# Optimization experiments

Measured on AMD Instinct MI355X. Metric: run time of the kernel, lower is better.

The kernel has to match this reference:

```python
import jax, jax.numpy as jnp
import numpy as np

HEAD_NUM = 16
MASK_FILL = 100000.0  # source uses +1e5 on masked entries (not -inf)


def setup_inputs() -> dict:
    key = jax.random.key(0)
    k1, k2, k3, k4, k5 = jax.random.split(key, 5)
    B, S, E = 2, 2048, 1024
    scale = 0.02
    return {
        "x": jax.random.normal(k1, (B, S, E), dtype=jnp.float32),
        "W_atten": jax.random.normal(k2, (E, 3 * E), dtype=jnp.float32) * scale,
        "b_atten": jax.random.normal(k3, (3 * E,), dtype=jnp.float32) * scale,
        "W_proj": jax.random.normal(k4, (E, E), dtype=jnp.float32) * scale,
        "b_proj": jax.random.normal(k5, (E,), dtype=jnp.float32) * scale,
    }


def reference(x, W_atten, b_atten, W_proj, b_proj):
    B, S, E = x.shape
    H = HEAD_NUM
    hd = E // H
    # QKV projection: [B, S, 3E]
    qkv = x @ W_atten + b_atten
    # reshape [B, S, H, 3*hd] -> [B, H, S, 3*hd], chunk into q,k,v [B,H,S,hd]
    qkv = jnp.transpose(qkv.reshape(B, S, H, 3 * hd), (0, 2, 1, 3))
    q, k, v = jnp.split(qkv, 3, axis=-1)
    # raw scores, NO 1/sqrt(dk) scaling (faithful to source)
    w = jnp.einsum("bhqd,bhkd->bhqk", q, k)
    # causal mask applied as w*mask + (1-mask)*1e5 (faithful to source)
    mask = jnp.tril(jnp.ones((S, S), dtype=w.dtype))
    w = w * mask + (1.0 - mask) * MASK_FILL
    # softmax over dim=1 == HEAD axis (faithful to source quirk)
    w = jax.nn.softmax(w, axis=1)
    # attn_drop: identity in eval mode
    a = jnp.einsum("bhqk,bhkd->bhqd", w, v)  # [B,H,S,hd]
    a = jnp.transpose(a, (0, 2, 1, 3)).reshape(B, S, E)
    h = a @ W_proj + b_proj
    # resi_drop: identity in eval mode
    return h
```

## Files before the change

### kernel.cpp

```cpp
#include <hip/hip_runtime.h>

#define DI __device__ __forceinline__

typedef __attribute__((ext_vector_type(8))) short s16x8;
typedef __attribute__((ext_vector_type(4))) short s16x4;
typedef __attribute__((ext_vector_type(4))) float f32x4;

DI unsigned short f2bf(float f){
  unsigned u = __float_as_uint(f);
  u = (u + 0x7FFFu + ((u >> 16) & 1u)) >> 16;
  return (unsigned short)u;
}
DI float bf2f(unsigned short h){
  return __uint_as_float(((unsigned)h) << 16);
}
DI float exp2i(float x){ float r; asm("v_exp_f32 %0, %1" : "=v"(r) : "v"(x)); return r; }

DI void gll16(const void* g, void* l){
  __builtin_amdgcn_global_load_lds((const __attribute__((address_space(1))) void*)g,
                                   (__attribute__((address_space(3))) void*)l, 16, 0, 0);
}

#define VMCNT(n) asm volatile("s_waitcnt vmcnt(" #n ")" ::: "memory")
#define SB() __builtin_amdgcn_sched_barrier(0)

__global__ void prep_kernel(const float* __restrict__ x, unsigned short* __restrict__ xb,
                            const float* __restrict__ Wa, unsigned short* __restrict__ WaT,
                            const float* __restrict__ Wp, unsigned short* __restrict__ WpT)
{
  __shared__ float t[32][33];
  int blk = blockIdx.x, tid = threadIdx.x;
  if (blk < 2048){
    int i = blk * 256 + tid;
    const float4* p = (const float4*)x + (size_t)i * 2;
    float4 a = p[0], b = p[1];
    s16x8 o;
    o[0] = (short)f2bf(a.x); o[1] = (short)f2bf(a.y); o[2] = (short)f2bf(a.z); o[3] = (short)f2bf(a.w);
    o[4] = (short)f2bf(b.x); o[5] = (short)f2bf(b.y); o[6] = (short)f2bf(b.z); o[7] = (short)f2bf(b.w);
    ((s16x8*)xb)[i] = o;
  } else {
    const float* in; unsigned short* out; int R, C, bx, by;
    if (blk < 5120){
      int k = blk - 2048; in = Wa; out = WaT; R = 1024; C = 3072; bx = k % 96; by = k / 96;
    } else {
      int k = blk - 5120; in = Wp; out = WpT; R = 1024; C = 1024; bx = k % 32; by = k / 32;
    }
    int c0 = bx * 32, r0 = by * 32;
    int tx = tid & 31, ty = tid >> 5;
    #pragma unroll
    for (int i = 0; i < 4; i++)
      t[ty + i*8][tx] = in[(size_t)(r0 + ty + i*8) * C + c0 + tx];
    __syncthreads();
    #pragma unroll
    for (int i = 0; i < 4; i++)
      out[(size_t)(c0 + ty + i*8) * R + r0 + tx] = f2bf(t[tx][ty + i*8]);
  }
}

template<int MODE, int BM>
__launch_bounds__(256)
__global__ void gemm_kernel(const unsigned short* __restrict__ A,
                            const unsigned short* __restrict__ Wt,
                            const float* __restrict__ bias,
                            int N,
                            unsigned short* __restrict__ qb,
                            unsigned short* __restrict__ kb,
                            unsigned short* __restrict__ vt,
                            float* __restrict__ out)
{
  constexpr int MI = BM / 32;
  constexpr int AC = BM / 32;
  const int K = 1024;
  __shared__ __align__(16) unsigned short Sm[BM*64 + 128*64];
  unsigned short* As = Sm;
  unsigned short* Bs = Sm + BM*64;

  int lin = blockIdx.y * gridDim.x + blockIdx.x;
  int chunk = (gridDim.x * gridDim.y) >> 3;
  int v = (lin & 7) * chunk + (lin >> 3);
  int bx = v % gridDim.x, by = v / gridDim.x;
  int m0 = by * BM, n0 = bx * 128;

  int tid = threadIdx.x;
  int lane = tid & 63, w = tid >> 6;
  int row_l = lane & 15, kgrp = lane >> 4;
  int wm = (w >> 1) * (MI * 16), wn = (w & 1) * 64;

  const unsigned short* asrc[AC];
  const unsigned short* bsrc[4];
  int ldsoA[AC], ldsoB[4];
  int chnk = (lane & 7) ^ (lane >> 3);
  #pragma unroll
  for (int c4 = 0; c4 < AC; c4++){
    int r = c4*32 + w*8 + (lane >> 3);
    asrc[c4] = A + (size_t)(m0 + r) * K + chnk*8;
    ldsoA[c4] = (c4*32 + w*8) * 64;
  }
  #pragma unroll
  for (int c4 = 0; c4 < 4; c4++){
    int r = c4*32 + w*8 + (lane >> 3);
    bsrc[c4] = Wt + (size_t)(n0 + r) * K + chnk*8;
    ldsoB[c4] = (c4*32 + w*8) * 64;
  }
  int eA[MI], eB[4];
  #pragma unroll
  for (int i = 0; i < MI; i++){
    int ra = wm + i*16 + row_l;
    eA[i] = (ra*64 + kgrp*8) ^ ((ra & 7) << 3);
  }
  #pragma unroll
  for (int i = 0; i < 4; i++){
    int rb = wn + i*16 + row_l;
    eB[i] = (rb*64 + kgrp*8) ^ ((rb & 7) << 3);
  }

  f32x4 acc[MI][4];
  #pragma unroll
  for (int i = 0; i < MI; i++)
    #pragma unroll
    for (int j = 0; j < 4; j++)
      acc[i][j] = (f32x4){0.f, 0.f, 0.f, 0.f};

  for (int k0 = 0; k0 < K; k0 += 64){
    #pragma unroll
    for (int c4 = 0; c4 < AC; c4++)
      gll16(asrc[c4] + k0, (void*)(As + ldsoA[c4]));
    #pragma unroll
    for (int c4 = 0; c4 < 4; c4++)
      gll16(bsrc[c4] + k0, (void*)(Bs + ldsoB[c4]));
    __syncthreads();
    #pragma unroll
    for (int kc = 0; kc < 2; kc++){
      s16x8 af[MI], bfr[4];
      #pragma unroll
      for (int mi = 0; mi < MI; mi++)
        af[mi] = *(const s16x8*)&As[eA[mi] ^ (kc*32)];
      #pragma unroll
      for (int ni = 0; ni < 4; ni++)
        bfr[ni] = *(const s16x8*)&Bs[eB[ni] ^ (kc*32)];
      #pragma unroll
      for (int mi = 0; mi < MI; mi++)
        #pragma unroll
        for (int ni = 0; ni < 4; ni++)
          acc[mi][ni] = __builtin_amdgcn_mfma_f32_16x16x32_bf16(af[mi], bfr[ni], acc[mi][ni], 0, 0, 0);
    }
    __syncthreads();
  }

  if (MODE == 0){
    constexpr int WU = BM / 4;
    constexpr int SWM = BM / 16 - 1;
    unsigned long long* ldsT = (unsigned long long*)Sm;
    #pragma unroll
    for (int mi = 0; mi < MI; mi++){
      #pragma unroll
      for (int ni = 0; ni < 4; ni++){
        int np = wn + ni*16 + row_l;
        int gc = n0 + np;
        int hh = gc / 192, cc = gc % 192;
        float bia = bias[gc];
        if (cc < 128){
          #pragma unroll
          for (int j = 0; j < 4; j++){
            int gr = m0 + wm + mi*16 + kgrp*4 + j;
            float v2 = acc[mi][ni][j] + bia;
            if (cc < 64){
              qb[(size_t)gr * 1024 + hh*64 + cc] = f2bf(v2 * 1.44269504f);
            } else {
              int d = cc - 64; int b = gr >> 11, s = gr & 2047;
              int kt = s >> 6, kk = s & 63;
              kb[(size_t)((b*16 + hh)*32 + kt) * 4096 + ((kk*64 + d) ^ ((kk & 7) << 3))] = f2bf(v2);
            }
          }
        } else {
          float v0 = acc[mi][ni][0] + bia, v1 = acc[mi][ni][1] + bia;
          float v2 = acc[mi][ni][2] + bia, v3 = acc[mi][ni][3] + bia;
          unsigned lo, hi;
          asm("v_cvt_pk_bf16_f32 %0, %1, %2" : "=v"(lo) : "v"(v0), "v"(v1));
          asm("v_cvt_pk_bf16_f32 %0, %1, %2" : "=v"(hi) : "v"(v2), "v"(v3));
          int mq = (wm + mi*16 + kgrp*4) >> 2;
          ldsT[np*WU + (mq ^ ((np & SWM) << 2))] = ((unsigned long long)hi << 32) | (unsigned long long)lo;
        }
      }
    }
    __syncthreads();
    constexpr int SUBS = BM / 64;
    constexpr int ITEMS = 128 * SUBS * 8;
    int bb = m0 >> 11, s_base = m0 & 2047;
    for (int item = tid; item < ITEMS; item += 256){
      int np = item / (SUBS * 8);
      int rem = item - np * (SUBS * 8);
      int sub = rem >> 3;
      int c = rem & 7;
      int gcv = n0 + np;
      int cc = gcv % 192;
      if (cc < 128) continue;
      int d = cc - 128, hh = gcv / 192;
      int mq0 = sub*16 + c*2;
      s16x8 val = *(const s16x8*)&Sm[np*BM + ((mq0 ^ ((np & SWM) << 2)) << 2)];
      size_t base = ((size_t)((bb*16 + hh)*32) + (s_base >> 6) + sub) * 4096 + d*64 + ((c ^ (d & 7)) << 3);
      *(s16x8*)&vt[base] = val;
    }
  } else {
    #pragma unroll
    for (int mi = 0; mi < MI; mi++){
      #pragma unroll
      for (int ni = 0; ni < 4; ni++){
        #pragma unroll
        for (int j = 0; j < 4; j++){
          int gr = m0 + wm + mi*16 + kgrp*4 + j;
          int gc = n0 + wn + ni*16 + row_l;
          out[(size_t)gr * N + gc] = acc[mi][ni][j] + bias[gc];
        }
      }
    }
  }
}

__global__ void sufv_kernel(const unsigned short* __restrict__ vt, float* __restrict__ sufv){
  __shared__ float tot[4][64];
  int bh = blockIdx.x;
  int tid = threadIdx.x;
  int tq = tid >> 6, d = tid & 63;
  const unsigned short* base = vt + (size_t)bh * 32 * 4096;
  float s[8];
  float run = 0.f;
  for (int j = 7; j >= 0; j--){
    int t = tq*8 + j;
    float rs = 0.f;
    #pragma unroll
    for (int c = 0; c < 8; c++){
      int idx = (d*64 + c*8) ^ ((d & 7) << 3);
      s16x8 v = *(const s16x8*)&base[(size_t)t*4096 + idx];
      #pragma unroll
      for (int e = 0; e < 8; e++) rs += bf2f((unsigned short)v[e]);
    }
    run += rs; s[j] = run;
  }
  tot[tq][d] = run;
  __syncthreads();
  float carry = 0.f;
  for (int t2 = tq+1; t2 < 4; t2++) carry += tot[t2][d];
  #pragma unroll
  for (int j = 0; j < 8; j++)
    sufv[((size_t)bh*33 + tq*8 + j)*64 + d] = s[j] + carry;
  if (tid < 64) sufv[((size_t)bh*33 + 32)*64 + tid] = 0.f;
}

__launch_bounds__(256)
__global__ void dpass_kernel(const unsigned short* __restrict__ qbuf,
                             const unsigned short* __restrict__ kb,
                             unsigned short* __restrict__ invb)
{
  __shared__ unsigned short Kst[4][4096];
  int bid = blockIdx.x;
  int blk = (bid & 7) * 132 + (bid >> 3);
  int b = blk / 528, t0 = blk % 528;
  int kt = (int)(32.5f - sqrtf(1056.25f - 2.f*t0));
  while (kt*(65-kt)/2 > t0) kt--;
  while ((kt+1)*(64-kt)/2 <= t0) kt++;
  int qt = kt + (t0 - kt*(65-kt)/2);

  int tid = threadIdx.x, lane = tid & 63, w = tid >> 6;
  int row_l = lane & 15, kgrp = lane >> 4;

  const unsigned short* ktb = kb + ((size_t)(b*16)*32 + kt) * 4096;
  int sgoff = (w*128 + lane)*8;

  auto stage = [&](int hh){
    const unsigned short* src = ktb + (size_t)hh * 131072;
    gll16(src + sgoff,       (void*)(&Kst[hh & 3][0] + w*1024));
    gll16(src + sgoff + 512, (void*)(&Kst[hh & 3][0] + w*1024 + 512));
  };

  int e0[4];
  #pragma unroll
  for (int ks = 0; ks < 4; ks++){
    int row = ks*16 + row_l;
    e0[ks] = (row*64 + kgrp*8) ^ ((row & 7) << 3);
  }

  const unsigned short* qrow_p = qbuf + (size_t)(b*2048 + qt*64 + w*16 + row_l) * 1024;

  stage(0); stage(1);
  s16x8 qa0 = *(const s16x8*)&qrow_p[kgrp*8];
  s16x8 qa1 = *(const s16x8*)&qrow_p[32 + kgrp*8];
  s16x8 qb0 = *(const s16x8*)&qrow_p[64 + kgrp*8];
  s16x8 qb1 = *(const s16x8*)&qrow_p[64 + 32 + kgrp*8];
  SB();

  f32x4 esum[4];
  #pragma unroll
  for (int ks = 0; ks < 4; ks++) esum[ks] = (f32x4){0.f,0.f,0.f,0.f};

  for (int t = 0; t < 8; t++){
    int h = 2*t;
    s16x8 qn0, qn1, qn2, qn3;
    if (t < 7){
      qn0 = *(const s16x8*)&qrow_p[(h+2)*64 + kgrp*8];
      qn1 = *(const s16x8*)&qrow_p[(h+2)*64 + 32 + kgrp*8];
      qn2 = *(const s16x8*)&qrow_p[(h+3)*64 + kgrp*8];
      qn3 = *(const s16x8*)&qrow_p[(h+3)*64 + 32 + kgrp*8];
    }
    SB();
    if (t == 0)     VMCNT(8);
    else if (t < 7) VMCNT(4);
    else            VMCNT(0);
    SB();
    __builtin_amdgcn_s_barrier();
    SB();
    if (t < 7){ stage(h+2); stage(h+3); }
    SB();

    const unsigned short* kl0 = &Kst[h & 3][0];
    const unsigned short* kl1 = &Kst[(h+1) & 3][0];
    #pragma unroll
    for (int ks = 0; ks < 4; ks++){
      s16x8 a0 = *(const s16x8*)&kl0[e0[ks]];
      s16x8 a1 = *(const s16x8*)&kl0[e0[ks] ^ 32];
      f32x4 sc = __builtin_amdgcn_mfma_f32_16x16x32_bf16(a0, qa0, (f32x4){0.f,0.f,0.f,0.f}, 0, 0, 0);
      sc = __builtin_amdgcn_mfma_f32_16x16x32_bf16(a1, qa1, sc, 0, 0, 0);
      s16x8 b0 = *(const s16x8*)&kl1[e0[ks]];
      s16x8 b1 = *(const s16x8*)&kl1[e0[ks] ^ 32];
      f32x4 sd = __builtin_amdgcn_mfma_f32_16x16x32_bf16(b0, qb0, (f32x4){0.f,0.f,0.f,0.f}, 0, 0, 0);
      sd = __builtin_amdgcn_mfma_f32_16x16x32_bf16(b1, qb1, sd, 0, 0, 0);
      #pragma unroll
      for (int j = 0; j < 4; j++) esum[ks][j] += exp2i(sc[j]) + exp2i(sd[j]);
    }
    if (t < 7){ qa0 = qn0; qa1 = qn1; qb0 = qn2; qb1 = qn3; }
  }

  int qcol = qt*64 + w*16 + row_l;
  unsigned short* dst = invb + (size_t)b*4194304 + (size_t)qcol*2048 + kt*64 + kgrp*4;
  #pragma unroll
  for (int ks = 0; ks < 4; ks++){
    float r0 = 1.f/esum[ks][0], r1 = 1.f/esum[ks][1];
    float r2 = 1.f/esum[ks][2], r3 = 1.f/esum[ks][3];
    unsigned lo, hi;
    asm("v_cvt_pk_bf16_f32 %0, %1, %2" : "=v"(lo) : "v"(r0), "v"(r1));
    asm("v_cvt_pk_bf16_f32 %0, %1, %2" : "=v"(hi) : "v"(r2), "v"(r3));
    uint2 pk; pk.x = lo; pk.y = hi;
    *(uint2*)&dst[ks*16] = pk;
  }
}

__launch_bounds__(256)
__global__ void pv_kernel(const unsigned short* __restrict__ qbuf,
                          const unsigned short* __restrict__ kb,
                          const unsigned short* __restrict__ vt,
                          const unsigned short* __restrict__ invb,
                          const float* __restrict__ sufv,
                          unsigned short* __restrict__ ab)
{
  __shared__ unsigned short Kst[3][4096];
  __shared__ unsigned short Vst[2][4096];
  __shared__ unsigned short Wsh[4][1152];

  int bid = blockIdx.x;
  int blk = ((bid & 7) << 6) | (bid >> 3);
  int i = blk & 15;
  int h = (blk >> 4) & 15;
  int b = blk >> 8;

  int tid = threadIdx.x, lane = tid & 63, w = tid >> 6;
  int row_l = lane & 15, kgrp = lane >> 4;

  const unsigned short* KT = kb + (size_t)((b*16 + h)*32) * 4096;
  const unsigned short* VT = vt + (size_t)((b*16 + h)*32) * 4096;
  int sgoff = (w*128 + lane)*8;
  unsigned short* Wsw = &Wsh[w][0];

  int eK[4];
  #pragma unroll
  for (int ks = 0; ks < 4; ks++){
    int row = ks*16 + row_l;
    eK[ks] = (row*64 + kgrp*8) ^ ((row & 7) << 3);
  }

  auto stageK = [&](int kt, int buf){
    gll16(KT + (size_t)kt*4096 + sgoff,       (void*)(&Kst[buf][0] + w*1024));
    gll16(KT + (size_t)kt*4096 + sgoff + 512, (void*)(&Kst[buf][0] + w*1024 + 512));
  };
  auto stageV = [&](int kt, int buf){
    gll16(VT + (size_t)kt*4096 + sgoff,       (void*)(&Vst[buf][0] + w*1024));
    gll16(VT + (size_t)kt*4096 + sgoff + 512, (void*)(&Vst[buf][0] + w*1024 + 512));
  };

  auto run = [&](int qt, int k1t){
    int q0 = qt * 64;
    int qv = q0 + w*16 + row_l;
    const unsigned short* qrow_p = qbuf + (size_t)(b*2048 + qv) * 1024 + h*64;
    s16x8 qf0 = *(const s16x8*)&qrow_p[kgrp*8];
    s16x8 qf1 = *(const s16x8*)&qrow_p[32 + kgrp*8];
    SB();
    const unsigned short* ivrow = invb + (size_t)b*4194304 + (size_t)qv*2048 + kgrp*4;

    f32x4 pvv[4];
    #pragma unroll
    for (int d = 0; d < 4; d++) pvv[d] = (f32x4){0.f,0.f,0.f,0.f};

    __syncthreads();
    stageK(0, 0);
    stageV(0, 0);
    s16x4 i1[4];
    #pragma unroll
    for (int ks = 0; ks < 4; ks++) i1[ks] = *(const s16x4*)&ivrow[ks*16];
    if (1 < k1t) stageK(1, 1);
    SB();

    for (int kt = 0; kt < k1t; kt++){
      bool nx1 = (kt + 1 < k1t), nx2 = (kt + 2 < k1t);
      bool first = (kt == 0);

      s16x4 icur[4];
      #pragma unroll
      for (int ks = 0; ks < 4; ks++) icur[ks] = i1[ks];
      if (nx1){
        #pragma unroll
        for (int ks = 0; ks < 4; ks++) i1[ks] = *(const s16x4*)&ivrow[(kt+1)*64 + ks*16];
      }
      SB();
      if (first){
        if (nx1) VMCNT(10);
        else     VMCNT(4);
      } else {
        if (nx1) VMCNT(6);
        else     VMCNT(0);
      }
      SB();
      __builtin_amdgcn_s_barrier();
      SB();
      if (nx1) stageV(kt+1, (kt+1) & 1);
      if (nx2) stageK(kt+2, (kt+2) % 3);
      SB();

      const unsigned short* kl = &Kst[kt % 3][0];
      const unsigned short* vl = &Vst[kt & 1][0];
      f32x4 sc[4];
      __builtin_amdgcn_s_setprio(1);
      #pragma unroll
      for (int ks = 0; ks < 4; ks++){
        s16x8 a0 = *(const s16x8*)&kl[eK[ks]];
        s16x8 a1 = *(const s16x8*)&kl[eK[ks] ^ 32];
        sc[ks] = __builtin_amdgcn_mfma_f32_16x16x32_bf16(a0, qf0, (f32x4){0.f,0.f,0.f,0.f}, 0, 0, 0);
        sc[ks] = __builtin_amdgcn_mfma_f32_16x16x32_bf16(a1, qf1, sc[ks], 0, 0, 0);
      }
      __builtin_amdgcn_s_setprio(0);

      if (kt == qt){
        int kbase = kt*64 + kgrp*4;
        #pragma unroll
        for (int ks = 0; ks < 4; ks++){
          #pragma unroll
          for (int j = 0; j < 4; j++){
            float wv = exp2i(sc[ks][j]) * bf2f((unsigned short)icur[ks][j]);
            sc[ks][j] = (kbase + ks*16 + j > qv) ? 0.0625f : wv;
          }
          unsigned lo, hi;
          asm("v_cvt_pk_bf16_f32 %0, %1, %2" : "=v"(lo) : "v"(sc[ks][0]), "v"(sc[ks][1]));
          asm("v_cvt_pk_bf16_f32 %0, %1, %2" : "=v"(hi) : "v"(sc[ks][2]), "v"(sc[ks][3]));
          uint2 pk2; pk2.x = lo; pk2.y = hi;
          *(uint2*)&Wsw[row_l*72 + ks*16 + kgrp*4] = pk2;
        }
      } else {
        #pragma unroll
        for (int ks = 0; ks < 4; ks++){
          #pragma unroll
          for (int j = 0; j < 4; j++)
            sc[ks][j] = exp2i(sc[ks][j]) * bf2f((unsigned short)icur[ks][j]);
          unsigned lo, hi;
          asm("v_cvt_pk_bf16_f32 %0, %1, %2" : "=v"(lo) : "v"(sc[ks][0]), "v"(sc[ks][1]));
          asm("v_cvt_pk_bf16_f32 %0, %1, %2" : "=v"(hi) : "v"(sc[ks][2]), "v"(sc[ks][3]));
          uint2 pk2; pk2.x = lo; pk2.y = hi;
          *(uint2*)&Wsw[row_l*72 + ks*16 + kgrp*4] = pk2;
        }
      }

      __builtin_amdgcn_s_setprio(1);
      #pragma unroll
      for (int kc = 0; kc < 2; kc++){
        s16x8 af = *(const s16x8*)&Wsw[row_l*72 + kc*32 + kgrp*8];
        #pragma unroll
        for (int dq = 0; dq < 4; dq++){
          s16x8 vf = *(const s16x8*)&vl[eK[dq] ^ (kc*32)];
          pvv[dq] = __builtin_amdgcn_mfma_f32_16x16x32_bf16(af, vf, pvv[dq], 0, 0, 0);
        }
      }
      __builtin_amdgcn_s_setprio(0);
    }

    int tsuf = qt + 1;
    #pragma unroll
    for (int dq = 0; dq < 4; dq++){
      int d = dq*16 + row_l;
      float suf = sufv[((size_t)(b*16 + h)*33 + tsuf)*64 + d];
      #pragma unroll
      for (int j = 0; j < 4; j++){
        int qo = q0 + w*16 + kgrp*4 + j;
        ab[(size_t)(b*2048 + qo)*1024 + h*64 + d] = f2bf(pvv[dq][j] + 0.0625f * suf);
      }
    }
  };

  run(i, i + 1);
  run(31 - i, 32 - i);
}

extern "C" void kernel_launch(void* const* d_in, const int* in_sizes, int n_in,
                              void* d_out, int out_size, void* d_ws, size_t ws_size,
                              hipStream_t stream) {
  (void)in_sizes; (void)n_in; (void)out_size; (void)ws_size;
  const float* x  = (const float*)d_in[0];
  const float* Wa = (const float*)d_in[1];
  const float* ba = (const float*)d_in[2];
  const float* Wp = (const float*)d_in[3];
  const float* bp = (const float*)d_in[4];
  float* out = (float*)d_out;

  char* ws = (char*)d_ws;
  size_t off = 0;
  auto alloc = [&](size_t bytes) -> void* {
    void* p = ws + off;
    off += (bytes + 255) & ~(size_t)255;
    return p;
  };
  unsigned short* xb   = (unsigned short*)alloc((size_t)4096*1024*2);
  unsigned short* WaT  = (unsigned short*)alloc((size_t)3072*1024*2);
  unsigned short* WpT  = (unsigned short*)alloc((size_t)1024*1024*2);
  unsigned short* qbuf = (unsigned short*)alloc((size_t)4096*1024*2);
  unsigned short* ktile= (unsigned short*)alloc((size_t)4096*1024*2);
  unsigned short* vtile= (unsigned short*)alloc((size_t)4096*1024*2);
  unsigned short* abuf = (unsigned short*)alloc((size_t)4096*1024*2);
  unsigned short* invb = (unsigned short*)alloc((size_t)2*2048*2048*2);
  float* sufv          = (float*)alloc((size_t)32*33*64*4);

  prep_kernel<<<6144, 256, 0, stream>>>(x, xb, Wa, WaT, Wp, WpT);

  gemm_kernel<0,64><<<dim3(24, 64), 256, 0, stream>>>(xb, WaT, ba, 3072, qbuf, ktile, vtile, nullptr);

  sufv_kernel<<<32, 256, 0, stream>>>(vtile, sufv);

  dpass_kernel<<<1056, 256, 0, stream>>>(qbuf, ktile, invb);

  pv_kernel<<<512, 256, 0, stream>>>(qbuf, ktile, vtile, invb, sufv, abuf);

  gemm_kernel<1,32><<<dim3(8, 128), 256, 0, stream>>>(abuf, WpT, bp, 1024, nullptr, nullptr, nullptr, out);
}
```

Before: 148.3 us.

## Process paired query tiles in one K/V sweep to share staged tiles

Each block previously ran two separate passes over K/V, one for query tile i and one for the mirrored tile 31-i, staging K and V tiles into shared memory twice. The passes are now merged into a single loop over 32-i key tiles. Each staged K/V tile is used by both query tiles while the short tile is still active, which cuts the global-to-LDS traffic and the pipeline restarts. In exchange each thread holds two sets of Q fragments and accumulators, which raises register pressure, and the vmcnt wait counts were retuned to cover the extra inverse-factor loads.

```diff
diff --git a/kernel.cpp b/kernel.cpp
--- a/kernel.cpp
+++ b/kernel.cpp
@@ -386,124 +386,151 @@
     gll16(VT + (size_t)kt*4096 + sgoff + 512, (void*)(&Vst[buf][0] + w*1024 + 512));
   };
 
-  auto run = [&](int qt, int k1t){
-    int q0 = qt * 64;
-    int qv = q0 + w*16 + row_l;
-    const unsigned short* qrow_p = qbuf + (size_t)(b*2048 + qv) * 1024 + h*64;
-    s16x8 qf0 = *(const s16x8*)&qrow_p[kgrp*8];
-    s16x8 qf1 = *(const s16x8*)&qrow_p[32 + kgrp*8];
-    SB();
-    const unsigned short* ivrow = invb + (size_t)b*4194304 + (size_t)qv*2048 + kgrp*4;
-
-    f32x4 pvv[4];
-    #pragma unroll
-    for (int d = 0; d < 4; d++) pvv[d] = (f32x4){0.f,0.f,0.f,0.f};
-
-    __syncthreads();
-    stageK(0, 0);
-    stageV(0, 0);
-    s16x4 i1[4];
-    #pragma unroll
-    for (int ks = 0; ks < 4; ks++) i1[ks] = *(const s16x4*)&ivrow[ks*16];
-    if (1 < k1t) stageK(1, 1);
-    SB();
-
-    for (int kt = 0; kt < k1t; kt++){
-      bool nx1 = (kt + 1 < k1t), nx2 = (kt + 2 < k1t);
-      bool first = (kt == 0);
-
-      s16x4 icur[4];
-      #pragma unroll
-      for (int ks = 0; ks < 4; ks++) icur[ks] = i1[ks];
-      if (nx1){
+  int qtA = i, qtB = 31 - i;
+  int k1t = 32 - i;
+  int qvA = qtA*64 + w*16 + row_l;
+  int qvB = qtB*64 + w*16 + row_l;
+  const unsigned short* qrowA = qbuf + (size_t)(b*2048 + qvA) * 1024 + h*64;
+  const unsigned short* qrowB = qbuf + (size_t)(b*2048 + qvB) * 1024 + h*64;
+  s16x8 qfA0 = *(const s16x8*)&qrowA[kgrp*8];
+  s16x8 qfA1 = *(const s16x8*)&qrowA[32 + kgrp*8];
+  s16x8 qfB0 = *(const s16x8*)&qrowB[kgrp*8];
+  s16x8 qfB1 = *(const s16x8*)&qrowB[32 + kgrp*8];
+  SB();
+  const unsigned short* ivA = invb + (size_t)b*4194304 + (size_t)qvA*2048 + kgrp*4;
+  const unsigned short* ivB = invb + (size_t)b*4194304 + (size_t)qvB*2048 + kgrp*4;
+
+  f32x4 pvA[4], pvB[4];
+  #pragma unroll
+  for (int d = 0; d < 4; d++){ pvA[d] = (f32x4){0.f,0.f,0.f,0.f}; pvB[d] = (f32x4){0.f,0.f,0.f,0.f}; }
+
+  auto compute_tile = [&](int kt, const unsigned short* kl, const unsigned short* vl,
+                          s16x8 qf0, s16x8 qf1, int qt, int qv, s16x4* icur, f32x4* pvv){
+    f32x4 sc[4];
+    __builtin_amdgcn_s_setprio(1);
+    #pragma unroll
+    for (int ks = 0; ks < 4; ks++){
+      s16x8 a0 = *(const s16x8*)&kl[eK[ks]];
+      s16x8 a1 = *(const s16x8*)&kl[eK[ks] ^ 32];
+      sc[ks] = __builtin_amdgcn_mfma_f32_16x16x32_bf16(a0, qf0, (f32x4){0.f,0.f,0.f,0.f}, 0, 0, 0);
+      sc[ks] = __builtin_amdgcn_mfma_f32_16x16x32_bf16(a1, qf1, sc[ks], 0, 0, 0);
+    }
+    __builtin_amdgcn_s_setprio(0);
+    if (kt == qt){
+      int kbase = kt*64 + kgrp*4;
+      #pragma unroll
+      for (int ks = 0; ks < 4; ks++){
         #pragma unroll
-        for (int ks = 0; ks < 4; ks++) i1[ks] = *(const s16x4*)&ivrow[(kt+1)*64 + ks*16];
-      }
-      SB();
-      if (first){
-        if (nx1) VMCNT(10);
-        else     VMCNT(4);
-      } else {
-        if (nx1) VMCNT(6);
-        else     VMCNT(0);
-      }
-      SB();
-      __builtin_amdgcn_s_barrier();
-      SB();
-      if (nx1) stageV(kt+1, (kt+1) & 1);
-      if (nx2) stageK(kt+2, (kt+2) % 3);
-      SB();
-
-      const unsigned short* kl = &Kst[kt % 3][0];
-      const unsigned short* vl = &Vst[kt & 1][0];
-      f32x4 sc[4];
-      __builtin_amdgcn_s_setprio(1);
+        for (int j = 0; j < 4; j++){
+          float wv = exp2i(sc[ks][j]) * bf2f((unsigned short)icur[ks][j]);
+          sc[ks][j] = (kbase + ks*16 + j > qv) ? 0.0625f : wv;
+        }
+        unsigned lo, hi;
+        asm("v_cvt_pk_bf16_f32 %0, %1, %2" : "=v"(lo) : "v"(sc[ks][0]), "v"(sc[ks][1]));
+        asm("v_cvt_pk_bf16_f32 %0, %1, %2" : "=v"(hi) : "v"(sc[ks][2]), "v"(sc[ks][3]));
+        uint2 pk2; pk2.x = lo; pk2.y = hi;
+        *(uint2*)&Wsw[row_l*72 + ks*16 + kgrp*4] = pk2;
+      }
+    } else {
       #pragma unroll
       for (int ks = 0; ks < 4; ks++){
-        s16x8 a0 = *(const s16x8*)&kl[eK[ks]];
-        s16x8 a1 = *(const s16x8*)&kl[eK[ks] ^ 32];
-        sc[ks] = __builtin_amdgcn_mfma_f32_16x16x32_bf16(a0, qf0, (f32x4){0.f,0.f,0.f,0.f}, 0, 0, 0);
-        sc[ks] = __builtin_amdgcn_mfma_f32_16x16x32_bf16(a1, qf1, sc[ks], 0, 0, 0);
-      }
-      __builtin_amdgcn_s_setprio(0);
-
-      if (kt == qt){
-        int kbase = kt*64 + kgrp*4;
         #pragma unroll
-        for (int ks = 0; ks < 4; ks++){
-          #pragma unroll
-          for (int j = 0; j < 4; j++){
-            float wv = exp2i(sc[ks][j]) * bf2f((unsigned short)icur[ks][j]);
-            sc[ks][j] = (kbase + ks*16 + j > qv) ? 0.0625f : wv;
-          }
-          unsigned lo, hi;
-          asm("v_cvt_pk_bf16_f32 %0, %1, %2" : "=v"(lo) : "v"(sc[ks][0]), "v"(sc[ks][1]));
-          asm("v_cvt_pk_bf16_f32 %0, %1, %2" : "=v"(hi) : "v"(sc[ks][2]), "v"(sc[ks][3]));
-          uint2 pk2; pk2.x = lo; pk2.y = hi;
-          *(uint2*)&Wsw[row_l*72 + ks*16 + kgrp*4] = pk2;
-        }
-      } else {
-        #pragma unroll
-        for (int ks = 0; ks < 4; ks++){
-          #pragma unroll
-          for (int j = 0; j < 4; j++)
-            sc[ks][j] = exp2i(sc[ks][j]) * bf2f((unsigned short)icur[ks][j]);
-          unsigned lo, hi;
-          asm("v_cvt_pk_bf16_f32 %0, %1, %2" : "=v"(lo) : "v"(sc[ks][0]), "v"(sc[ks][1]));
-          asm("v_cvt_pk_bf16_f32 %0, %1, %2" : "=v"(hi) : "v"(sc[ks][2]), "v"(sc[ks][3]));
-          uint2 pk2; pk2.x = lo; pk2.y = hi;
-          *(uint2*)&Wsw[row_l*72 + ks*16 + kgrp*4] = pk2;
-        }
-      }
-
-      __builtin_amdgcn_s_setprio(1);
-      #pragma unroll
-      for (int kc = 0; kc < 2; kc++){
-        s16x8 af = *(const s16x8*)&Wsw[row_l*72 + kc*32 + kgrp*8];
-        #pragma unroll
-        for (int dq = 0; dq < 4; dq++){
-          s16x8 vf = *(const s16x8*)&vl[eK[dq] ^ (kc*32)];
-          pvv[dq] = __builtin_amdgcn_mfma_f32_16x16x32_bf16(af, vf, pvv[dq], 0, 0, 0);
-        }
-      }
-      __builtin_amdgcn_s_setprio(0);
-    }
-
-    int tsuf = qt + 1;
+        for (int j = 0; j < 4; j++)
+          sc[ks][j] = exp2i(sc[ks][j]) * bf2f((unsigned short)icur[ks][j]);
+        unsigned lo, hi;
+        asm("v_cvt_pk_bf16_f32 %0, %1, %2" : "=v"(lo) : "v"(sc[ks][0]), "v"(sc[ks][1]));
+        asm("v_cvt_pk_bf16_f32 %0, %1, %2" : "=v"(hi) : "v"(sc[ks][2]), "v"(sc[ks][3]));
+        uint2 pk2; pk2.x = lo; pk2.y = hi;
+        *(uint2*)&Wsw[row_l*72 + ks*16 + kgrp*4] = pk2;
+      }
+    }
+    __builtin_amdgcn_s_setprio(1);
+    #pragma unroll
+    for (int kc = 0; kc < 2; kc++){
+      s16x8 af = *(const s16x8*)&Wsw[row_l*72 + kc*32 + kgrp*8];
+      #pragma unroll
+      for (int dq = 0; dq < 4; dq++){
+        s16x8 vf = *(const s16x8*)&vl[eK[dq] ^ (kc*32)];
+        pvv[dq] = __builtin_amdgcn_mfma_f32_16x16x32_bf16(af, vf, pvv[dq], 0, 0, 0);
+      }
+    }
+    __builtin_amdgcn_s_setprio(0);
+  };
+
+  stageK(0, 0);
+  stageV(0, 0);
+  s16x4 iA1[4], iB1[4];
+  #pragma unroll
+  for (int ks = 0; ks < 4; ks++){
+    iA1[ks] = *(const s16x4*)&ivA[ks*16];
+    iB1[ks] = *(const s16x4*)&ivB[ks*16];
+  }
+  stageK(1, 1);
+  SB();
+
+  for (int kt = 0; kt < k1t; kt++){
+    bool cA  = (kt <= qtA);
+    bool nxA = (kt + 1 <= qtA);
+    bool nx1 = (kt + 1 < k1t), nx2 = (kt + 2 < k1t);
+    bool first = (kt == 0);
+
+    s16x4 icA[4], icB[4];
+    #pragma unroll
+    for (int ks = 0; ks < 4; ks++){ icA[ks] = iA1[ks]; icB[ks] = iB1[ks]; }
+    if (nxA){
+      #pragma unroll
+      for (int ks = 0; ks < 4; ks++) iA1[ks] = *(const s16x4*)&ivA[(kt+1)*64 + ks*16];
+    }
+    if (nx1){
+      #pragma unroll
+      for (int ks = 0; ks < 4; ks++) iB1[ks] = *(const s16x4*)&ivB[(kt+1)*64 + ks*16];
+    }
+    SB();
+    if (first){
+      if (nxA) VMCNT(18);
+      else     VMCNT(14);
+    } else {
+      if (nxA)      VMCNT(10);
+      else if (nx1) VMCNT(6);
+      else          VMCNT(0);
+    }
+    SB();
+    __builtin_amdgcn_s_barrier();
+    SB();
+    if (nx1) stageV(kt+1, (kt+1) & 1);
+    if (nx2) stageK(kt+2, (kt+2) % 3);
+    SB();
+
+    const unsigned short* kl = &Kst[kt % 3][0];
+    const unsigned short* vl = &Vst[kt & 1][0];
+    compute_tile(kt, kl, vl, qfB0, qfB1, qtB, qvB, icB, pvB);
+    if (cA) compute_tile(kt, kl, vl, qfA0, qfA1, qtA, qvA, icA, pvA);
+  }
+
+  {
+    int tsufA = qtA + 1;
     #pragma unroll
     for (int dq = 0; dq < 4; dq++){
       int d = dq*16 + row_l;
-      float suf = sufv[((size_t)(b*16 + h)*33 + tsuf)*64 + d];
+      float suf = sufv[((size_t)(b*16 + h)*33 + tsufA)*64 + d];
       #pragma unroll
       for (int j = 0; j < 4; j++){
-        int qo = q0 + w*16 + kgrp*4 + j;
-        ab[(size_t)(b*2048 + qo)*1024 + h*64 + d] = f2bf(pvv[dq][j] + 0.0625f * suf);
-      }
-    }
-  };
-
-  run(i, i + 1);
-  run(31 - i, 32 - i);
+        int qo = qtA*64 + w*16 + kgrp*4 + j;
+        ab[(size_t)(b*2048 + qo)*1024 + h*64 + d] = f2bf(pvA[dq][j] + 0.0625f * suf);
+      }
+    }
+    int tsufB = qtB + 1;
+    #pragma unroll
+    for (int dq = 0; dq < 4; dq++){
+      int d = dq*16 + row_l;
+      float suf = sufv[((size_t)(b*16 + h)*33 + tsufB)*64 + d];
+      #pragma unroll
+      for (int j = 0; j < 4; j++){
+        int qo = qtB*64 + w*16 + kgrp*4 + j;
+        ab[(size_t)(b*2048 + qo)*1024 + h*64 + d] = f2bf(pvB[dq][j] + 0.0625f * suf);
+      }
+    }
+  }
 }
 
 extern "C" void kernel_launch(void* const* d_in, const int* in_sizes, int n_in,
```

New measurement: 156.2 us. 1.05x slower.

## Split paired q-tiles into separate blocks and shrink pv_kernel LDS staging

Applied to the files above, without the earlier changes.

The PV kernel no longer runs two balanced query tiles (i and 31-i) per block. It launches 1024 blocks, one query tile each, with an XCD-aware mapping so that blocks sharing a batch/head land on the same XCD. K staging drops from triple to double buffering, loaded together with V one tile ahead, and the W scratch uses an XOR swizzle instead of row padding. Smaller LDS and more blocks aim to raise occupancy and parallelism. The cost is possible load imbalance across blocks and less prefetch depth for K.

```diff
diff --git a/kernel.cpp b/kernel.cpp
--- a/kernel.cpp
+++ b/kernel.cpp
@@ -352,15 +352,17 @@
                           const float* __restrict__ sufv,
                           unsigned short* __restrict__ ab)
 {
-  __shared__ unsigned short Kst[3][4096];
+  __shared__ unsigned short Kst[2][4096];
   __shared__ unsigned short Vst[2][4096];
-  __shared__ unsigned short Wsh[4][1152];
+  __shared__ unsigned short Wsh[4][1024];
 
   int bid = blockIdx.x;
-  int blk = ((bid & 7) << 6) | (bid >> 3);
-  int i = blk & 15;
-  int h = (blk >> 4) & 15;
-  int b = blk >> 8;
+  int xcd = bid & 7, s = bid >> 3;
+  int g = s & 31, r = s >> 5;
+  int B = xcd*4 + r;
+  int b = B >> 4, h = B & 15;
+  int qt = (r & 1) ? (31 - g) : g;
+  int k1t = qt + 1;
 
   int tid = threadIdx.x, lane = tid & 63, w = tid >> 6;
   int row_l = lane & 15, kgrp = lane >> 4;
@@ -369,6 +371,7 @@
   const unsigned short* VT = vt + (size_t)((b*16 + h)*32) * 4096;
   int sgoff = (w*128 + lane)*8;
   unsigned short* Wsw = &Wsh[w][0];
+  int xw = (row_l & 7) << 3;
 
   int eK[4];
   #pragma unroll
@@ -386,124 +389,119 @@
     gll16(VT + (size_t)kt*4096 + sgoff + 512, (void*)(&Vst[buf][0] + w*1024 + 512));
   };
 
-  auto run = [&](int qt, int k1t){
-    int q0 = qt * 64;
-    int qv = q0 + w*16 + row_l;
-    const unsigned short* qrow_p = qbuf + (size_t)(b*2048 + qv) * 1024 + h*64;
-    s16x8 qf0 = *(const s16x8*)&qrow_p[kgrp*8];
-    s16x8 qf1 = *(const s16x8*)&qrow_p[32 + kgrp*8];
-    SB();
-    const unsigned short* ivrow = invb + (size_t)b*4194304 + (size_t)qv*2048 + kgrp*4;
-
-    f32x4 pvv[4];
-    #pragma unroll
-    for (int d = 0; d < 4; d++) pvv[d] = (f32x4){0.f,0.f,0.f,0.f};
-
-    __syncthreads();
-    stageK(0, 0);
-    stageV(0, 0);
-    s16x4 i1[4];
-    #pragma unroll
-    for (int ks = 0; ks < 4; ks++) i1[ks] = *(const s16x4*)&ivrow[ks*16];
-    if (1 < k1t) stageK(1, 1);
-    SB();
-
-    for (int kt = 0; kt < k1t; kt++){
-      bool nx1 = (kt + 1 < k1t), nx2 = (kt + 2 < k1t);
-      bool first = (kt == 0);
-
-      s16x4 icur[4];
-      #pragma unroll
-      for (int ks = 0; ks < 4; ks++) icur[ks] = i1[ks];
-      if (nx1){
+  int q0 = qt * 64;
+  int qv = q0 + w*16 + row_l;
+  const unsigned short* qrow_p = qbuf + (size_t)(b*2048 + qv) * 1024 + h*64;
+  s16x8 qf0 = *(const s16x8*)&qrow_p[kgrp*8];
+  s16x8 qf1 = *(const s16x8*)&qrow_p[32 + kgrp*8];
+  SB();
+  const unsigned short* ivrow = invb + (size_t)b*4194304 + (size_t)qv*2048 + kgrp*4;
+
+  f32x4 pvv[4];
+  #pragma unroll
+  for (int d = 0; d < 4; d++) pvv[d] = (f32x4){0.f,0.f,0.f,0.f};
+
+  stageK(0, 0);
+  stageV(0, 0);
+  s16x4 i1[4];
+  #pragma unroll
+  for (int ks = 0; ks < 4; ks++) i1[ks] = *(const s16x4*)&ivrow[ks*16];
+  SB();
+
+  for (int kt = 0; kt < k1t; kt++){
+    bool nx1 = (kt + 1 < k1t);
+    bool first = (kt == 0);
+
+    s16x4 icur[4];
+    #pragma unroll
+    for (int ks = 0; ks < 4; ks++) icur[ks] = i1[ks];
+    if (nx1){
+      #pragma unroll
+      for (int ks = 0; ks < 4; ks++) i1[ks] = *(const s16x4*)&ivrow[(kt+1)*64 + ks*16];
+    }
+    SB();
+    if (first){
+      if (nx1) VMCNT(8);
+      else     VMCNT(4);
+    } else {
+      if (nx1) VMCNT(4);
+      else     VMCNT(0);
+    }
+    SB();
+    __builtin_amdgcn_s_barrier();
+    SB();
+    if (nx1){
+      stageV(kt+1, (kt+1) & 1);
+      stageK(kt+1, (kt+1) & 1);
+    }
+    SB();
+
+    const unsigned short* kl = &Kst[kt & 1][0];
+    const unsigned short* vl = &Vst[kt & 1][0];
+    f32x4 sc[4];
+    __builtin_amdgcn_s_setprio(1);
+    #pragma unroll
+    for (int ks = 0; ks < 4; ks++){
+      s16x8 a0 = *(const s16x8*)&kl[eK[ks]];
+      s16x8 a1 = *(const s16x8*)&kl[eK[ks] ^ 32];
+      sc[ks] = __builtin_amdgcn_mfma_f32_16x16x32_bf16(a0, qf0, (f32x4){0.f,0.f,0.f,0.f}, 0, 0, 0);
+      sc[ks] = __builtin_amdgcn_mfma_f32_16x16x32_bf16(a1, qf1, sc[ks], 0, 0, 0);
+    }
+    __builtin_amdgcn_s_setprio(0);
+
+    if (kt == qt){
+      int kbase = kt*64 + kgrp*4;
+      #pragma unroll
+      for (int ks = 0; ks < 4; ks++){
         #pragma unroll
-        for (int ks = 0; ks < 4; ks++) i1[ks] = *(const s16x4*)&ivrow[(kt+1)*64 + ks*16];
+        for (int j = 0; j < 4; j++){
+          float wv = exp2i(sc[ks][j]) * bf2f((unsigned short)icur[ks][j]);
+          sc[ks][j] = (kbase + ks*16 + j > qv) ? 0.0625f : wv;
+        }
+        unsigned lo, hi;
+        asm("v_cvt_pk_bf16_f32 %0, %1, %2" : "=v"(lo) : "v"(sc[ks][0]), "v"(sc[ks][1]));
+        asm("v_cvt_pk_bf16_f32 %0, %1, %2" : "=v"(hi) : "v"(sc[ks][2]), "v"(sc[ks][3]));
+        uint2 pk2; pk2.x = lo; pk2.y = hi;
+        *(uint2*)&Wsw[row_l*64 + ((ks*16 + kgrp*4) ^ xw)] = pk2;
       }
-      SB();
-      if (first){
-        if (nx1) VMCNT(10);
-        else     VMCNT(4);
-      } else {
-        if (nx1) VMCNT(6);
-        else     VMCNT(0);
+    } else {
+      #pragma unroll
+      for (int ks = 0; ks < 4; ks++){
+        #pragma unroll
+        for (int j = 0; j < 4; j++)
+          sc[ks][j] = exp2i(sc[ks][j]) * bf2f((unsigned short)icur[ks][j]);
+        unsigned lo, hi;
+        asm("v_cvt_pk_bf16_f32 %0, %1, %2" : "=v"(lo) : "v"(sc[ks][0]), "v"(sc[ks][1]));
+        asm("v_cvt_pk_bf16_f32 %0, %1, %2" : "=v"(hi) : "v"(sc[ks][2]), "v"(sc[ks][3]));
+        uint2 pk2; pk2.x = lo; pk2.y = hi;
+        *(uint2*)&Wsw[row_l*64 + ((ks*16 + kgrp*4) ^ xw)] = pk2;
       }
-      SB();
-      __builtin_amdgcn_s_barrier();
-      SB();
-      if (nx1) stageV(kt+1, (kt+1) & 1);
-      if (nx2) stageK(kt+2, (kt+2) % 3);
-      SB();
-
-      const unsigned short* kl = &Kst[kt % 3][0];
-      const unsigned short* vl = &Vst[kt & 1][0];
-      f32x4 sc[4];
-      __builtin_amdgcn_s_setprio(1);
-      #pragma unroll
-      for (int ks = 0; ks < 4; ks++){
-        s16x8 a0 = *(const s16x8*)&kl[eK[ks]];
-        s16x8 a1 = *(const s16x8*)&kl[eK[ks] ^ 32];
-        sc[ks] = __builtin_amdgcn_mfma_f32_16x16x32_bf16(a0, qf0, (f32x4){0.f,0.f,0.f,0.f}, 0, 0, 0);
-        sc[ks] = __builtin_amdgcn_mfma_f32_16x16x32_bf16(a1, qf1, sc[ks], 0, 0, 0);
+    }
+
+    __builtin_amdgcn_s_setprio(1);
+    #pragma unroll
+    for (int kc = 0; kc < 2; kc++){
+      s16x8 af = *(const s16x8*)&Wsw[row_l*64 + ((kc*32 + kgrp*8) ^ xw)];
+      #pragma unroll
+      for (int dq = 0; dq < 4; dq++){
+        s16x8 vf = *(const s16x8*)&vl[eK[dq] ^ (kc*32)];
+        pvv[dq] = __builtin_amdgcn_mfma_f32_16x16x32_bf16(af, vf, pvv[dq], 0, 0, 0);
       }
-      __builtin_amdgcn_s_setprio(0);
-
-      if (kt == qt){
-        int kbase = kt*64 + kgrp*4;
-        #pragma unroll
-        for (int ks = 0; ks < 4; ks++){
-          #pragma unroll
-          for (int j = 0; j < 4; j++){
-            float wv = exp2i(sc[ks][j]) * bf2f((unsigned short)icur[ks][j]);
-            sc[ks][j] = (kbase + ks*16 + j > qv) ? 0.0625f : wv;
-          }
-          unsigned lo, hi;
-          asm("v_cvt_pk_bf16_f32 %0, %1, %2" : "=v"(lo) : "v"(sc[ks][0]), "v"(sc[ks][1]));
-          asm("v_cvt_pk_bf16_f32 %0, %1, %2" : "=v"(hi) : "v"(sc[ks][2]), "v"(sc[ks][3]));
-          uint2 pk2; pk2.x = lo; pk2.y = hi;
-          *(uint2*)&Wsw[row_l*72 + ks*16 + kgrp*4] = pk2;
-        }
-      } else {
-        #pragma unroll
-        for (int ks = 0; ks < 4; ks++){
-          #pragma unroll
-          for (int j = 0; j < 4; j++)
-            sc[ks][j] = exp2i(sc[ks][j]) * bf2f((unsigned short)icur[ks][j]);
-          unsigned lo, hi;
-          asm("v_cvt_pk_bf16_f32 %0, %1, %2" : "=v"(lo) : "v"(sc[ks][0]), "v"(sc[ks][1]));
-          asm("v_cvt_pk_bf16_f32 %0, %1, %2" : "=v"(hi) : "v"(sc[ks][2]), "v"(sc[ks][3]));
-          uint2 pk2; pk2.x = lo; pk2.y = hi;
-          *(uint2*)&Wsw[row_l*72 + ks*16 + kgrp*4] = pk2;
-        }
-      }
-
-      __builtin_amdgcn_s_setprio(1);
-      #pragma unroll
-      for (int kc = 0; kc < 2; kc++){
-        s16x8 af = *(const s16x8*)&Wsw[row_l*72 + kc*32 + kgrp*8];
-        #pragma unroll
-        for (int dq = 0; dq < 4; dq++){
-          s16x8 vf = *(const s16x8*)&vl[eK[dq] ^ (kc*32)];
-          pvv[dq] = __builtin_amdgcn_mfma_f32_16x16x32_bf16(af, vf, pvv[dq], 0, 0, 0);
-        }
-      }
-      __builtin_amdgcn_s_setprio(0);
-    }
-
-    int tsuf = qt + 1;
-    #pragma unroll
-    for (int dq = 0; dq < 4; dq++){
-      int d = dq*16 + row_l;
-      float suf = sufv[((size_t)(b*16 + h)*33 + tsuf)*64 + d];
-      #pragma unroll
-      for (int j = 0; j < 4; j++){
-        int qo = q0 + w*16 + kgrp*4 + j;
-        ab[(size_t)(b*2048 + qo)*1024 + h*64 + d] = f2bf(pvv[dq][j] + 0.0625f * suf);
-      }
-    }
-  };
-
-  run(i, i + 1);
-  run(31 - i, 32 - i);
+    }
+    __builtin_amdgcn_s_setprio(0);
+  }
+
+  int tsuf = qt + 1;
+  #pragma unroll
+  for (int dq = 0; dq < 4; dq++){
+    int d = dq*16 + row_l;
+    float suf = sufv[((size_t)(b*16 + h)*33 + tsuf)*64 + d];
+    #pragma unroll
+    for (int j = 0; j < 4; j++){
+      int qo = q0 + w*16 + kgrp*4 + j;
+      ab[(size_t)(b*2048 + qo)*1024 + h*64 + d] = f2bf(pvv[dq][j] + 0.0625f * suf);
+    }
+  }
 }
 
 extern "C" void kernel_launch(void* const* d_in, const int* in_sizes, int n_in,
@@ -542,7 +540,7 @@
 
   dpass_kernel<<<1056, 256, 0, stream>>>(qbuf, ktile, invb);
 
-  pv_kernel<<<512, 256, 0, stream>>>(qbuf, ktile, vtile, invb, sufv, abuf);
+  pv_kernel<<<1024, 256, 0, stream>>>(qbuf, ktile, vtile, invb, sufv, abuf);
 
   gemm_kernel<1,32><<<dim3(8, 128), 256, 0, stream>>>(abuf, WpT, bp, 1024, nullptr, nullptr, nullptr, out);
 }
```

Result: slower. 153.7 us (+3.6%).
